# Kernel tuning notes

Measured on AMD Instinct MI355X. Metric: run time of the kernel, lower is better.

Reference implementation:

```python
import jax, jax.numpy as jnp
import numpy as np

BLOCK = 8
HALO = 3
HEADS = 8
DIM_HEAD = 64
DIM = 128
MAX_NEG = -3.402823466e38  # -torch.finfo(float32).max, matches the CUDA kernel


def _extract_patches(xp, nh, nw, block, K):
    # xp: [b, c, Hp, Wp] (already padded). Returns [b, c, nh, nw, K, K]
    ih = (jnp.arange(nh) * block)[:, None] + jnp.arange(K)[None, :]  # [nh, K]
    iw = (jnp.arange(nw) * block)[:, None] + jnp.arange(K)[None, :]  # [nw, K]
    return xp[..., ih[:, None, :, None], iw[None, :, None, :]]


def setup_inputs() -> dict:
    key = jax.random.key(0)
    k1, k2, k3, k4, k5 = jax.random.split(key, 5)
    inner = HEADS * DIM_HEAD
    x = jax.random.normal(k1, (4, DIM, 128, 128), dtype=jnp.float32)
    s = 1.0 / np.sqrt(DIM)
    Wq = jax.random.normal(k2, (DIM, inner), dtype=jnp.float32) * s
    Wkv = jax.random.normal(k3, (DIM, 2 * inner), dtype=jnp.float32) * s
    Wo = jax.random.normal(k4, (inner, DIM), dtype=jnp.float32) * (1.0 / np.sqrt(inner))
    bo = jax.random.normal(k5, (DIM,), dtype=jnp.float32) * 0.01
    return {"x": x, "Wq": Wq, "Wkv": Wkv, "Wo": Wo, "bo": bo}


def reference(x, Wq, Wkv, Wo, bo):
    b, c, h, w = x.shape
    block, halo, heads, dh = BLOCK, HALO, HEADS, DIM_HEAD
    K = block + 2 * halo
    nh, nw = h // block, w // block
    nb = nh * nw
    I, J = block * block, K * K
    scale = dh ** -0.5

    # queries per block: [b, nb, I, c]
    q_inp = (x.reshape(b, c, nh, block, nw, block)
              .transpose(0, 2, 4, 3, 5, 1)
              .reshape(b, nb, I, c))

    # halo key/value windows via unfold-equivalent patch extraction
    xp = jnp.pad(x, ((0, 0), (0, 0), (halo, halo), (halo, halo)))
    kv = _extract_patches(xp, nh, nw, block, K)           # [b, c, nh, nw, K, K]
    kv_inp = kv.transpose(0, 2, 3, 4, 5, 1).reshape(b, nb, J, c)

    # mask: True where the halo window overlaps padding
    ones = jnp.pad(jnp.ones((1, 1, h, w), x.dtype),
                   ((0, 0), (0, 0), (halo, halo), (halo, halo)))
    mask = (_extract_patches(ones, nh, nw, block, K).reshape(nb, J) == 0)

    q = (q_inp @ Wq).reshape(b, nb, I, heads, dh) * scale
    kvp = kv_inp @ Wkv                                    # [b, nb, J, 2*inner]
    inner = heads * dh
    k = kvp[..., :inner].reshape(b, nb, J, heads, dh)
    v = kvp[..., inner:].reshape(b, nb, J, heads, dh)

    sim = jnp.einsum('bnihd,bnjhd->bnhij', q, k)          # [b, nb, heads, I, J]
    sim = jnp.where(mask[None, :, None, None, :], MAX_NEG, sim)
    attn = jax.nn.softmax(sim, axis=-1)
    out = jnp.einsum('bnhij,bnjhd->bnihd', attn, v)       # [b, nb, I, heads, dh]

    out = out.reshape(b, nb, I, inner) @ Wo + bo          # [b, nb, I, c]
    out = (out.reshape(b, nh, nw, block, block, c)
              .transpose(0, 5, 1, 3, 2, 4)
              .reshape(b, c, h, w))
    return out
```

## Files before the change

kernel.cpp:

```cpp
#include <hip/hip_runtime.h>
#include <hip/hip_bf16.h>

typedef unsigned short u16;
typedef __attribute__((ext_vector_type(8))) short short8;
typedef __attribute__((ext_vector_type(16))) float f32x16;
typedef __attribute__((ext_vector_type(2))) int int2v;

__device__ __forceinline__ u16 f2b(float f) {
    unsigned int u = __float_as_uint(f);
    return (u16)((u + 0x7fffu + ((u >> 16) & 1u)) >> 16);
}

__device__ __forceinline__ f32x16 zero16() {
    f32x16 z;
#pragma unroll
    for (int q = 0; q < 16; ++q) z[q] = 0.f;
    return z;
}

#define MFMA32(a, b, c) __builtin_amdgcn_mfma_f32_32x32x16_bf16((a), (b), (c), 0, 0, 0)

__global__ void prep_weights(const float* __restrict__ Wq,
                             const float* __restrict__ Wkv,
                             const float* __restrict__ Wo,
                             u16* __restrict__ ws)
{
    const int bid = blockIdx.x, tid = threadIdx.x;
    if (bid < 32) {
        __shared__ float wq_s[128 * 65];
        __shared__ float wk_s[32 * 65];
        const int h = bid >> 2, g = bid & 3;
        for (int i = tid; i < 8192; i += 256) {
            int c0 = i >> 6, d = i & 63;
            wq_s[c0 * 65 + d] = Wq[c0 * 512 + h * 64 + d];
        }
        for (int i = tid; i < 2048; i += 256) {
            int cl = i >> 6, d = i & 63;
            wk_s[cl * 65 + d] = Wkv[(g * 32 + cl) * 1024 + h * 64 + d];
        }
        __syncthreads();
        const int c0 = tid & 127, clb = (tid >> 7) * 16;
        float acc[16];
#pragma unroll
        for (int cc = 0; cc < 16; ++cc) acc[cc] = 0.f;
        for (int d = 0; d < 64; ++d) {
            float a = wq_s[c0 * 65 + d];
#pragma unroll
            for (int cc = 0; cc < 16; ++cc)
                acc[cc] = fmaf(a, wk_s[(clb + cc) * 65 + d], acc[cc]);
        }
#pragma unroll
        for (int cc = 0; cc < 16; ++cc)
            ws[h * 16384 + (g * 32 + clb + cc) * 128 + c0] = f2b(0.125f * acc[cc]);
    } else {
        int idx = (bid - 32) * 256 + tid;
        if (idx < 65536) {
            int h = idx >> 13, c = (idx >> 6) & 127, dv = idx & 63;
            ws[131072 + h * 8192 + dv * 128 + c] =
                f2b(Wkv[c * 1024 + 512 + h * 64 + dv]);
        } else {
            int j2 = idx - 65536;
            int cout = j2 >> 9, n = j2 & 511;
            ws[196608 + j2] = f2b(Wo[n * 128 + cout]);
        }
    }
}

__global__
__attribute__((amdgpu_flat_work_group_size(512, 512), amdgpu_waves_per_eu(2, 2)))
void halo_attn(const float* __restrict__ xg,
               const u16* __restrict__ wqk,
               const u16* __restrict__ wvt,
               const u16* __restrict__ wot,
               const float* __restrict__ bo,
               float* __restrict__ outg)
{
    extern __shared__ u16 lds[];
    u16* s_x  = lds;
    u16* t_sw = lds + 30464;
    u16* v_sw = lds + 39168;
    u16* p_sw = lds + 54016;
    u16* o_sw = lds + 68864;
    float* vmul = (float*)((char*)lds + 146944);

    const int tid  = threadIdx.x;
    const int w    = tid >> 6;
    const int lane = tid & 63;
    const int n5   = lane & 31;
    const int half = lane >> 5;

    const int wg = (blockIdx.x >> 3) + (blockIdx.x & 7) * 128;
    const int b   = wg >> 8;
    const int blk = wg & 255;
    const int by = blk >> 4, bx = blk & 15;
    const int y0 = by * 8 - 3, x0 = bx * 8 - 3;
    const bool inb = (by >= 1) && (by <= 14) && (bx >= 1) && (bx <= 14);

    for (int t = tid; t < 1904; t += 512)
        ((unsigned*)(s_x + 196 * 136))[t] = 0u;
    if (tid < 224) {
        int j = tid;
        float v = 0.f;
        if (j < 196) {
            int wy = j / 14, wx = j - wy * 14;
            if (inb || (((unsigned)(y0 + wy) < 128u) && ((unsigned)(x0 + wx) < 128u)))
                v = 1.f;
        }
        vmul[j] = v;
    }
    for (int idx = tid; idx < 32768; idx += 512) {
        int wx = idx & 15, wy = (idx >> 4) & 15, c = idx >> 8;
        if (wx < 14 && wy < 14) {
            int gy = y0 + wy, gx = x0 + wx;
            float val = 0.f;
            if (inb || (((unsigned)gy < 128u) && ((unsigned)gx < 128u)))
                val = xg[((b * 128 + c) * 128 + gy) * 128 + gx];
            s_x[(wy * 14 + wx) * 136 + c] = f2b(val);
        }
    }
    __syncthreads();

    const int ei = w & 1, c4 = w >> 1;
    const int i_t = ei * 32 + n5;
    const int jq  = ((i_t >> 3) + 3) * 14 + (i_t & 7) + 3;
    const int j7  = (w < 6) ? w : 6;
    const bool two = (w < 6);
    const int alt = (w == 7) ? 1 : 0;

    short8 xj[8];
#pragma unroll
    for (int kc = 0; kc < 8; ++kc)
        xj[kc] = *(const short8*)(s_x + (j7 * 32 + n5) * 136 + kc * 16 + half * 8);

    f32x16 res = zero16();
    const short os1 = (short)0x3F80;
    const short8 ones = {os1, os1, os1, os1, os1, os1, os1, os1};

#pragma unroll 1
    for (int h = 0; h < 8; ++h) {
        {
            f32x16 acc = zero16();
#pragma unroll
            for (int kc = 0; kc < 8; ++kc) {
                short8 a  = *(const short8*)(s_x + jq * 136 + kc * 16 + half * 8);
                short8 bq = *(const short8*)(wqk + h * 16384 +
                                             (c4 * 32 + n5) * 128 + kc * 16 + half * 8);
                acc = MFMA32(a, bq, acc);
            }
#pragma unroll
            for (int q = 0; q < 16; ++q) {
                int rq = (q & 3) + 8 * (q >> 2) + 4 * half;
                t_sw[(ei * 32 + rq) * 136 + c4 * 32 + n5] = f2b(acc[q]);
            }
        }
        {
            f32x16 va = zero16(), vb2 = zero16();
#pragma unroll
            for (int kc = 0; kc < 8; ++kc) {
                short8 b0 = *(const short8*)(wvt + h * 8192 +
                                             (alt * 32 + n5) * 128 + kc * 16 + half * 8);
                va = MFMA32(xj[kc], b0, va);
                if (two) {
                    short8 b1 = *(const short8*)(wvt + h * 8192 +
                                                 (32 + n5) * 128 + kc * 16 + half * 8);
                    vb2 = MFMA32(xj[kc], b1, vb2);
                }
            }
#pragma unroll
            for (int g = 0; g < 4; ++g) {
                unsigned lo = (unsigned)f2b(va[4 * g + 0]) |
                              ((unsigned)f2b(va[4 * g + 1]) << 16);
                unsigned hi = (unsigned)f2b(va[4 * g + 2]) |
                              ((unsigned)f2b(va[4 * g + 3]) << 16);
                int2v pk; pk[0] = (int)lo; pk[1] = (int)hi;
                *(int2v*)(v_sw + (alt * 32 + n5) * 232 + j7 * 32 + 8 * g + 4 * half) = pk;
            }
            if (two) {
#pragma unroll
                for (int g = 0; g < 4; ++g) {
                    unsigned lo = (unsigned)f2b(vb2[4 * g + 0]) |
                                  ((unsigned)f2b(vb2[4 * g + 1]) << 16);
                    unsigned hi = (unsigned)f2b(vb2[4 * g + 2]) |
                                  ((unsigned)f2b(vb2[4 * g + 3]) << 16);
                    int2v pk; pk[0] = (int)lo; pk[1] = (int)hi;
                    *(int2v*)(v_sw + (32 + n5) * 232 + j7 * 32 + 8 * g + 4 * half) = pk;
                }
            }
        }
        __syncthreads();

        {
            f32x16 sa = zero16(), sb = zero16();
#pragma unroll
            for (int kc = 0; kc < 8; ++kc) {
                short8 t0 = *(const short8*)(t_sw + (alt * 32 + n5) * 136 +
                                             kc * 16 + half * 8);
                sa = MFMA32(t0, xj[kc], sa);
                if (two) {
                    short8 t1 = *(const short8*)(t_sw + (32 + n5) * 136 +
                                                 kc * 16 + half * 8);
                    sb = MFMA32(t1, xj[kc], sb);
                }
            }
            const int j = j7 * 32 + n5;
            const float vm = vmul[j];
#pragma unroll
            for (int q = 0; q < 16; ++q) {
                int rq = (q & 3) + 8 * (q >> 2) + 4 * half;
                float p = __expf(sa[q]) * vm;
                p_sw[(alt * 32 + rq) * 232 + j] = f2b(p);
            }
            if (two) {
#pragma unroll
                for (int q = 0; q < 16; ++q) {
                    int rq = (q & 3) + 8 * (q >> 2) + 4 * half;
                    float p = __expf(sb[q]) * vm;
                    p_sw[(32 + rq) * 232 + j] = f2b(p);
                }
            }
        }
        __syncthreads();

        if (w < 4) {
            const int pi = w & 1, dv2 = w >> 1;
            f32x16 acc = zero16(), accs = zero16();
#pragma unroll
            for (int kc = 0; kc < 14; ++kc) {
                short8 pa = *(const short8*)(p_sw + (pi * 32 + n5) * 232 +
                                             kc * 16 + half * 8);
                short8 vb = *(const short8*)(v_sw + (dv2 * 32 + n5) * 232 +
                                             kc * 16 + half * 8);
                acc  = MFMA32(pa, vb, acc);
                accs = MFMA32(pa, ones, accs);
            }
#pragma unroll
            for (int q = 0; q < 16; ++q) {
                int rq = (q & 3) + 8 * (q >> 2) + 4 * half;
                int row = pi * 32 + rq;
                o_sw[row * 72 + dv2 * 32 + n5] = f2b(acc[q] / accs[q]);
            }
        }
        __syncthreads();

        {
#pragma unroll
            for (int kc = 0; kc < 4; ++kc) {
                short8 ao = *(const short8*)(o_sw + (ei * 32 + n5) * 72 +
                                             kc * 16 + half * 8);
                short8 bw = *(const short8*)(wot + (c4 * 32 + n5) * 512 + h * 64 +
                                             kc * 16 + half * 8);
                res = MFMA32(ao, bw, res);
            }
        }
    }

    {
        const int ch = c4 * 32 + n5;
        const float bias = bo[ch];
#pragma unroll
        for (int q = 0; q < 16; ++q) {
            int rq = (q & 3) + 8 * (q >> 2) + 4 * half;
            int i = ei * 32 + rq;
            int gy = by * 8 + (i >> 3), gx = bx * 8 + (i & 7);
            outg[((b * 128 + ch) * 128 + gy) * 128 + gx] = res[q] + bias;
        }
    }
}

extern "C" void kernel_launch(void* const* d_in, const int* in_sizes, int n_in,
                              void* d_out, int out_size, void* d_ws, size_t ws_size,
                              hipStream_t stream) {
    const float* x   = (const float*)d_in[0];
    const float* Wq  = (const float*)d_in[1];
    const float* Wkv = (const float*)d_in[2];
    const float* Wo  = (const float*)d_in[3];
    const float* bo  = (const float*)d_in[4];
    float* out = (float*)d_out;
    u16* ws = (u16*)d_ws;

    prep_weights<<<dim3(544), dim3(256), 0, stream>>>(Wq, Wkv, Wo, ws);

    (void)hipFuncSetAttribute((const void*)halo_attn,
                              hipFuncAttributeMaxDynamicSharedMemorySize, 147840);
    halo_attn<<<dim3(1024), dim3(512), 147840, stream>>>(
        x, ws, ws + 131072, ws + 196608, bo, out);
}
```

Baseline: 462.7 us.

## Assign one head per wave and keep attention in registers via permlane repacking

Restructures the attention kernel so each of the 8 waves owns one head and loops over key chunks. Scores, probabilities and V stay in registers, repacked between MFMA layouts with permlane32_swap instead of going through LDS. This removes the four per-head block barriers and the LDS round trips. All head outputs are staged in LDS once for a single final output projection. The trade-off is recomputing the Wqk-times-x product per key chunk and higher register pressure.

```diff
diff --git a/kernel.cpp b/kernel.cpp
--- a/kernel.cpp
+++ b/kernel.cpp
@@ -10,12 +10,33 @@
     unsigned int u = __float_as_uint(f);
     return (u16)((u + 0x7fffu + ((u >> 16) & 1u)) >> 16);
 }
-
+__device__ __forceinline__ unsigned pkbf(float a, float b) {
+    union { __hip_bfloat162 h; unsigned u; } cv;
+    cv.h = __float22bfloat162_rn(make_float2(a, b));
+    return cv.u;
+}
 __device__ __forceinline__ f32x16 zero16() {
     f32x16 z;
 #pragma unroll
     for (int q = 0; q < 16; ++q) z[q] = 0.f;
     return z;
+}
+__device__ __forceinline__ short8 mk8(unsigned w0, unsigned w1, unsigned w2, unsigned w3) {
+    union { unsigned u[4]; short8 s; } c;
+    c.u[0] = w0; c.u[1] = w1; c.u[2] = w2; c.u[3] = w3;
+    return c.s;
+}
+__device__ __forceinline__ void repack(const f32x16 a, short8& f0, short8& f1) {
+    unsigned x01 = pkbf(a[0], a[1]),  x23 = pkbf(a[2], a[3]);
+    unsigned x45 = pkbf(a[4], a[5]),  x67 = pkbf(a[6], a[7]);
+    auto r0 = __builtin_amdgcn_permlane32_swap((int)x01, (int)x45, false, false);
+    auto r1 = __builtin_amdgcn_permlane32_swap((int)x23, (int)x67, false, false);
+    f0 = mk8((unsigned)r0[0], (unsigned)r1[0], (unsigned)r0[1], (unsigned)r1[1]);
+    unsigned y01 = pkbf(a[8], a[9]),   y23 = pkbf(a[10], a[11]);
+    unsigned y45 = pkbf(a[12], a[13]), y67 = pkbf(a[14], a[15]);
+    auto s0 = __builtin_amdgcn_permlane32_swap((int)y01, (int)y45, false, false);
+    auto s1 = __builtin_amdgcn_permlane32_swap((int)y23, (int)y67, false, false);
+    f1 = mk8((unsigned)s0[0], (unsigned)s1[0], (unsigned)s0[1], (unsigned)s1[1]);
 }
 
 #define MFMA32(a, b, c) __builtin_amdgcn_mfma_f32_32x32x16_bf16((a), (b), (c), 0, 0, 0)
@@ -27,31 +48,31 @@
 {
     const int bid = blockIdx.x, tid = threadIdx.x;
     if (bid < 32) {
-        __shared__ float wq_s[128 * 65];
-        __shared__ float wk_s[32 * 65];
+        __shared__ float wk_f[128 * 65];
+        __shared__ float wq_g[32 * 65];
         const int h = bid >> 2, g = bid & 3;
         for (int i = tid; i < 8192; i += 256) {
-            int c0 = i >> 6, d = i & 63;
-            wq_s[c0 * 65 + d] = Wq[c0 * 512 + h * 64 + d];
+            int c = i >> 6, d = i & 63;
+            wk_f[c * 65 + d] = Wkv[c * 1024 + h * 64 + d];
         }
         for (int i = tid; i < 2048; i += 256) {
             int cl = i >> 6, d = i & 63;
-            wk_s[cl * 65 + d] = Wkv[(g * 32 + cl) * 1024 + h * 64 + d];
+            wq_g[cl * 65 + d] = Wq[(g * 32 + cl) * 512 + h * 64 + d];
         }
         __syncthreads();
-        const int c0 = tid & 127, clb = (tid >> 7) * 16;
+        const int bcol = tid & 127, clb = (tid >> 7) * 16;
         float acc[16];
 #pragma unroll
         for (int cc = 0; cc < 16; ++cc) acc[cc] = 0.f;
         for (int d = 0; d < 64; ++d) {
-            float a = wq_s[c0 * 65 + d];
+            float kb = wk_f[bcol * 65 + d];
 #pragma unroll
             for (int cc = 0; cc < 16; ++cc)
-                acc[cc] = fmaf(a, wk_s[(clb + cc) * 65 + d], acc[cc]);
+                acc[cc] = fmaf(kb, wq_g[(clb + cc) * 65 + d], acc[cc]);
         }
 #pragma unroll
         for (int cc = 0; cc < 16; ++cc)
-            ws[h * 16384 + (g * 32 + clb + cc) * 128 + c0] = f2b(0.125f * acc[cc]);
+            ws[h * 16384 + (g * 32 + clb + cc) * 128 + bcol] = f2b(0.125f * acc[cc]);
     } else {
         int idx = (bid - 32) * 256 + tid;
         if (idx < 65536) {
@@ -69,19 +90,17 @@
 __global__
 __attribute__((amdgpu_flat_work_group_size(512, 512), amdgpu_waves_per_eu(2, 2)))
 void halo_attn(const float* __restrict__ xg,
-               const u16* __restrict__ wqk,
+               const u16* __restrict__ wqk2,
                const u16* __restrict__ wvt,
                const u16* __restrict__ wot,
                const float* __restrict__ bo,
                float* __restrict__ outg)
 {
     extern __shared__ u16 lds[];
-    u16* s_x  = lds;
-    u16* t_sw = lds + 30464;
-    u16* v_sw = lds + 39168;
-    u16* p_sw = lds + 54016;
-    u16* o_sw = lds + 68864;
-    float* vmul = (float*)((char*)lds + 146944);
+    u16* s_x   = lds;
+    u16* o_all = lds + 30464;
+    unsigned* mask_l = (unsigned*)((char*)lds + 127488);
+    float* bo_l      = (float*)((char*)lds + 127520);
 
     const int tid  = threadIdx.x;
     const int w    = tid >> 6;
@@ -98,15 +117,18 @@
 
     for (int t = tid; t < 1904; t += 512)
         ((unsigned*)(s_x + 196 * 136))[t] = 0u;
-    if (tid < 224) {
-        int j = tid;
-        float v = 0.f;
-        if (j < 196) {
-            int wy = j / 14, wx = j - wy * 14;
-            if (inb || (((unsigned)(y0 + wy) < 128u) && ((unsigned)(x0 + wx) < 128u)))
-                v = 1.f;
-        }
-        vmul[j] = v;
+    if (tid < 128) bo_l[tid] = bo[tid];
+    if (tid < 7) {
+        unsigned m = 0;
+        for (int bp = 0; bp < 32; ++bp) {
+            int j = tid * 32 + bp;
+            if (j < 196) {
+                int wy = j / 14, wx = j - wy * 14;
+                if (inb || (((unsigned)(y0 + wy) < 128u) && ((unsigned)(x0 + wx) < 128u)))
+                    m |= (1u << bp);
+            }
+        }
+        mask_l[tid] = m;
     }
     for (int idx = tid; idx < 32768; idx += 512) {
         int wx = idx & 15, wy = (idx >> 4) & 15, c = idx >> 8;
@@ -120,149 +142,138 @@
     }
     __syncthreads();
 
-    const int ei = w & 1, c4 = w >> 1;
-    const int i_t = ei * 32 + n5;
-    const int jq  = ((i_t >> 3) + 3) * 14 + (i_t & 7) + 3;
-    const int j7  = (w < 6) ? w : 6;
-    const bool two = (w < 6);
-    const int alt = (w == 7) ? 1 : 0;
-
-    short8 xj[8];
-#pragma unroll
-    for (int kc = 0; kc < 8; ++kc)
-        xj[kc] = *(const short8*)(s_x + (j7 * 32 + n5) * 136 + kc * 16 + half * 8);
-
-    f32x16 res = zero16();
-    const short os1 = (short)0x3F80;
-    const short8 ones = {os1, os1, os1, os1, os1, os1, os1, os1};
+    const int h = w;
+    const int i0 = n5, i1 = 32 + n5;
+    const int jq0 = ((i0 >> 3) + 3) * 14 + (i0 & 7) + 3;
+    const int jq1 = ((i1 >> 3) + 3) * 14 + (i1 & 7) + 3;
+
+    f32x16 o00 = zero16(), o01 = zero16(), o10 = zero16(), o11 = zero16();
+    float sh0 = 0.f, sh1 = 0.f;
 
 #pragma unroll 1
-    for (int h = 0; h < 8; ++h) {
+    for (int j7 = 0; j7 < 7; ++j7) {
+        const unsigned msk = mask_l[j7];
+        short8 xj[8];
+#pragma unroll
+        for (int kc = 0; kc < 8; ++kc)
+            xj[kc] = *(const short8*)(s_x + (j7 * 32 + n5) * 136 + kc * 16 + half * 8);
+
+        f32x16 SC0 = zero16(), SC1 = zero16();
+        short8 cur[8], nxt[8];
+#pragma unroll
+        for (int kc = 0; kc < 8; ++kc)
+            cur[kc] = *(const short8*)(wqk2 + h * 16384 + n5 * 128 + kc * 16 + half * 8);
+#pragma unroll 1
+        for (int a4 = 0; a4 < 4; ++a4) {
+            if (a4 < 3) {
+#pragma unroll
+                for (int kc = 0; kc < 8; ++kc)
+                    nxt[kc] = *(const short8*)(wqk2 + h * 16384 +
+                               ((a4 + 1) * 32 + n5) * 128 + kc * 16 + half * 8);
+            }
+            f32x16 t2c = zero16();
+#pragma unroll
+            for (int kc = 0; kc < 8; ++kc) t2c = MFMA32(cur[kc], xj[kc], t2c);
+            short8 tA0, tA1;
+            repack(t2c, tA0, tA1);
+            short8 xb;
+            xb = *(const short8*)(s_x + jq0 * 136 + (a4 * 2 + 0) * 16 + half * 8);
+            SC0 = MFMA32(tA0, xb, SC0);
+            xb = *(const short8*)(s_x + jq0 * 136 + (a4 * 2 + 1) * 16 + half * 8);
+            SC0 = MFMA32(tA1, xb, SC0);
+            xb = *(const short8*)(s_x + jq1 * 136 + (a4 * 2 + 0) * 16 + half * 8);
+            SC1 = MFMA32(tA0, xb, SC1);
+            xb = *(const short8*)(s_x + jq1 * 136 + (a4 * 2 + 1) * 16 + half * 8);
+            SC1 = MFMA32(tA1, xb, SC1);
+#pragma unroll
+            for (int kc = 0; kc < 8; ++kc) cur[kc] = nxt[kc];
+        }
+
+        short8 pB00, pB01, pB10, pB11;
         {
-            f32x16 acc = zero16();
-#pragma unroll
-            for (int kc = 0; kc < 8; ++kc) {
-                short8 a  = *(const short8*)(s_x + jq * 136 + kc * 16 + half * 8);
-                short8 bq = *(const short8*)(wqk + h * 16384 +
-                                             (c4 * 32 + n5) * 128 + kc * 16 + half * 8);
-                acc = MFMA32(a, bq, acc);
-            }
+            f32x16 p0;
 #pragma unroll
             for (int q = 0; q < 16; ++q) {
-                int rq = (q & 3) + 8 * (q >> 2) + 4 * half;
-                t_sw[(ei * 32 + rq) * 136 + c4 * 32 + n5] = f2b(acc[q]);
-            }
-        }
-        {
-            f32x16 va = zero16(), vb2 = zero16();
-#pragma unroll
-            for (int kc = 0; kc < 8; ++kc) {
-                short8 b0 = *(const short8*)(wvt + h * 8192 +
-                                             (alt * 32 + n5) * 128 + kc * 16 + half * 8);
-                va = MFMA32(xj[kc], b0, va);
-                if (two) {
-                    short8 b1 = *(const short8*)(wvt + h * 8192 +
-                                                 (32 + n5) * 128 + kc * 16 + half * 8);
-                    vb2 = MFMA32(xj[kc], b1, vb2);
-                }
-            }
+                int rq = ((q & 3) + 8 * (q >> 2)) + 4 * half;
+                float e = __expf(SC0[q]);
+                p0[q] = ((msk >> rq) & 1u) ? e : 0.f;
+                sh0 += p0[q];
+            }
+            repack(p0, pB00, pB01);
+            f32x16 p1;
+#pragma unroll
+            for (int q = 0; q < 16; ++q) {
+                int rq = ((q & 3) + 8 * (q >> 2)) + 4 * half;
+                float e = __expf(SC1[q]);
+                p1[q] = ((msk >> rq) & 1u) ? e : 0.f;
+                sh1 += p1[q];
+            }
+            repack(p1, pB10, pB11);
+        }
+
+        short8 wv0[8], wv1[8];
+#pragma unroll
+        for (int kc = 0; kc < 8; ++kc) {
+            wv0[kc] = *(const short8*)(wvt + h * 8192 + n5 * 128 + kc * 16 + half * 8);
+            wv1[kc] = *(const short8*)(wvt + h * 8192 + (32 + n5) * 128 + kc * 16 + half * 8);
+        }
+        f32x16 vc0 = zero16(), vc1 = zero16();
+#pragma unroll
+        for (int kc = 0; kc < 8; ++kc) {
+            vc0 = MFMA32(xj[kc], wv0[kc], vc0);
+            vc1 = MFMA32(xj[kc], wv1[kc], vc1);
+        }
+        short8 vA00, vA01, vA10, vA11;
+        repack(vc0, vA00, vA01);
+        repack(vc1, vA10, vA11);
+
+        o00 = MFMA32(vA00, pB00, o00); o00 = MFMA32(vA01, pB01, o00);
+        o01 = MFMA32(vA00, pB10, o01); o01 = MFMA32(vA01, pB11, o01);
+        o10 = MFMA32(vA10, pB00, o10); o10 = MFMA32(vA11, pB01, o10);
+        o11 = MFMA32(vA10, pB10, o11); o11 = MFMA32(vA11, pB11, o11);
+    }
+
+    const float s0 = sh0 + __shfl_xor(sh0, 32);
+    const float s1 = sh1 + __shfl_xor(sh1, 32);
+    {
+        const f32x16* ot[4] = { &o00, &o01, &o10, &o11 };
+#pragma unroll
+        for (int t2i = 0; t2i < 4; ++t2i) {
+            const int i2 = t2i & 1, dv2 = t2i >> 1;
+            const float ss = i2 ? s1 : s0;
+            const f32x16 oa = *ot[t2i];
 #pragma unroll
             for (int g = 0; g < 4; ++g) {
-                unsigned lo = (unsigned)f2b(va[4 * g + 0]) |
-                              ((unsigned)f2b(va[4 * g + 1]) << 16);
-                unsigned hi = (unsigned)f2b(va[4 * g + 2]) |
-                              ((unsigned)f2b(va[4 * g + 3]) << 16);
+                unsigned lo = pkbf(oa[4 * g + 0] / ss, oa[4 * g + 1] / ss);
+                unsigned hi = pkbf(oa[4 * g + 2] / ss, oa[4 * g + 3] / ss);
                 int2v pk; pk[0] = (int)lo; pk[1] = (int)hi;
-                *(int2v*)(v_sw + (alt * 32 + n5) * 232 + j7 * 32 + 8 * g + 4 * half) = pk;
-            }
-            if (two) {
-#pragma unroll
-                for (int g = 0; g < 4; ++g) {
-                    unsigned lo = (unsigned)f2b(vb2[4 * g + 0]) |
-                                  ((unsigned)f2b(vb2[4 * g + 1]) << 16);
-                    unsigned hi = (unsigned)f2b(vb2[4 * g + 2]) |
-                                  ((unsigned)f2b(vb2[4 * g + 3]) << 16);
-                    int2v pk; pk[0] = (int)lo; pk[1] = (int)hi;
-                    *(int2v*)(v_sw + (32 + n5) * 232 + j7 * 32 + 8 * g + 4 * half) = pk;
-                }
-            }
-        }
-        __syncthreads();
-
-        {
-            f32x16 sa = zero16(), sb = zero16();
-#pragma unroll
-            for (int kc = 0; kc < 8; ++kc) {
-                short8 t0 = *(const short8*)(t_sw + (alt * 32 + n5) * 136 +
-                                             kc * 16 + half * 8);
-                sa = MFMA32(t0, xj[kc], sa);
-                if (two) {
-                    short8 t1 = *(const short8*)(t_sw + (32 + n5) * 136 +
-                                                 kc * 16 + half * 8);
-                    sb = MFMA32(t1, xj[kc], sb);
-                }
-            }
-            const int j = j7 * 32 + n5;
-            const float vm = vmul[j];
-#pragma unroll
-            for (int q = 0; q < 16; ++q) {
-                int rq = (q & 3) + 8 * (q >> 2) + 4 * half;
-                float p = __expf(sa[q]) * vm;
-                p_sw[(alt * 32 + rq) * 232 + j] = f2b(p);
-            }
-            if (two) {
-#pragma unroll
-                for (int q = 0; q < 16; ++q) {
-                    int rq = (q & 3) + 8 * (q >> 2) + 4 * half;
-                    float p = __expf(sb[q]) * vm;
-                    p_sw[(32 + rq) * 232 + j] = f2b(p);
-                }
-            }
-        }
-        __syncthreads();
-
-        if (w < 4) {
-            const int pi = w & 1, dv2 = w >> 1;
-            f32x16 acc = zero16(), accs = zero16();
-#pragma unroll
-            for (int kc = 0; kc < 14; ++kc) {
-                short8 pa = *(const short8*)(p_sw + (pi * 32 + n5) * 232 +
-                                             kc * 16 + half * 8);
-                short8 vb = *(const short8*)(v_sw + (dv2 * 32 + n5) * 232 +
-                                             kc * 16 + half * 8);
-                acc  = MFMA32(pa, vb, acc);
-                accs = MFMA32(pa, ones, accs);
-            }
-#pragma unroll
-            for (int q = 0; q < 16; ++q) {
-                int rq = (q & 3) + 8 * (q >> 2) + 4 * half;
-                int row = pi * 32 + rq;
-                o_sw[row * 72 + dv2 * 32 + n5] = f2b(acc[q] / accs[q]);
-            }
-        }
-        __syncthreads();
-
-        {
-#pragma unroll
-            for (int kc = 0; kc < 4; ++kc) {
-                short8 ao = *(const short8*)(o_sw + (ei * 32 + n5) * 72 +
-                                             kc * 16 + half * 8);
-                short8 bw = *(const short8*)(wot + (c4 * 32 + n5) * 512 + h * 64 +
-                                             kc * 16 + half * 8);
-                res = MFMA32(ao, bw, res);
-            }
-        }
-    }
+                *(int2v*)(o_all + (i2 * 32 + n5) * 520 +
+                          h * 64 + dv2 * 32 + 8 * g + 4 * half) = pk;
+            }
+        }
+    }
+    __syncthreads();
 
     {
-        const int ch = c4 * 32 + n5;
-        const float bias = bo[ch];
+        const int c4 = w >> 1, i2e = w & 1;
+        f32x16 e0 = zero16(), e1 = zero16();
+#pragma unroll 1
+        for (int kc = 0; kc < 32; kc += 2) {
+            short8 wa = *(const short8*)(wot + (c4 * 32 + n5) * 512 + kc * 16 + half * 8);
+            short8 ob = *(const short8*)(o_all + (i2e * 32 + n5) * 520 + kc * 16 + half * 8);
+            e0 = MFMA32(wa, ob, e0);
+            short8 wa2 = *(const short8*)(wot + (c4 * 32 + n5) * 512 + (kc + 1) * 16 + half * 8);
+            short8 ob2 = *(const short8*)(o_all + (i2e * 32 + n5) * 520 + (kc + 1) * 16 + half * 8);
+            e1 = MFMA32(wa2, ob2, e1);
+        }
+        const f32x16 res = e0 + e1;
+        const int i = i2e * 32 + n5;
+        const int gy = by * 8 + (i >> 3), gx = bx * 8 + (i & 7);
 #pragma unroll
         for (int q = 0; q < 16; ++q) {
-            int rq = (q & 3) + 8 * (q >> 2) + 4 * half;
-            int i = ei * 32 + rq;
-            int gy = by * 8 + (i >> 3), gx = bx * 8 + (i & 7);
-            outg[((b * 128 + ch) * 128 + gy) * 128 + gx] = res[q] + bias;
+            int rq = ((q & 3) + 8 * (q >> 2)) + 4 * half;
+            int ch = c4 * 32 + rq;
+            outg[((b * 128 + ch) * 128 + gy) * 128 + gx] = res[q] + bo_l[ch];
         }
     }
 }
@@ -281,7 +292,7 @@
     prep_weights<<<dim3(544), dim3(256), 0, stream>>>(Wq, Wkv, Wo, ws);
 
     (void)hipFuncSetAttribute((const void*)halo_attn,
-                              hipFuncAttributeMaxDynamicSharedMemorySize, 147840);
-    halo_attn<<<dim3(1024), dim3(512), 147840, stream>>>(
+                              hipFuncAttributeMaxDynamicSharedMemorySize, 128032);
+    halo_attn<<<dim3(1024), dim3(512), 128032, stream>>>(
         x, ws, ws + 131072, ws + 196608, bo, out);
 }
```

Result: slower. 609.1 us (+31.6%).
